# Performance work log

Measured on AMD Instinct MI355X. Metric: run time of the kernel, lower is better.

## Reference

```python
import jax, jax.numpy as jnp
import numpy as np

B = 32; H = 56; W = 56; C = 384; WS = 7; SHIFT = 3; NH = 12; HID = 1536; RANK = 192
N = WS * WS
NWIN = (H // WS) * (W // WS)


def _rel_index():
    coords = np.stack(np.meshgrid(np.arange(WS), np.arange(WS), indexing='ij')).reshape(2, -1)
    rel = (coords[:, :, None] - coords[:, None, :]).transpose(1, 2, 0)
    rel[..., 0] += WS - 1
    rel[..., 1] += WS - 1
    rel[..., 0] *= 2 * WS - 1
    return jnp.asarray(rel.sum(-1).reshape(-1))  # (N*N,) int


def _attn_mask():
    img = np.zeros((H, W))
    cnt = 0
    sls = (slice(0, -WS), slice(-WS, -SHIFT), slice(-SHIFT, None))
    for hs in sls:
        for ws_ in sls:
            img[hs, ws_] = cnt
            cnt += 1
    mw = img.reshape(H // WS, WS, W // WS, WS).transpose(0, 2, 1, 3).reshape(-1, N)
    am = mw[:, None, :] - mw[:, :, None]
    return jnp.asarray(np.where(am != 0, -100.0, 0.0).astype(np.float32))  # (nW,N,N)


REL_IDX = _rel_index()
ATTN_MASK = _attn_mask()


def _ln(x, g, b):
    m = x.mean(-1, keepdims=True)
    v = ((x - m) ** 2).mean(-1, keepdims=True)
    return (x - m) / jnp.sqrt(v + 1e-5) * g + b


def _flin(x, v, u, b):
    # FactorizedLinear: x @ V^T @ U^T + b
    return (x @ v.T) @ u.T + b


def setup_inputs() -> dict:
    key = jax.random.key(0)
    ks = jax.random.split(key, 12)
    def n(k, shape, s):
        return jax.random.normal(k, shape, jnp.float32) * s
    return {
        'x': jax.random.normal(ks[0], (B, H * W, C), jnp.float32),
        'norm1_g': jnp.ones((C,), jnp.float32), 'norm1_b': jnp.zeros((C,), jnp.float32),
        'rpb_table': n(ks[1], ((2 * WS - 1) ** 2, NH), 0.02),
        'qkv_v': n(ks[2], (RANK, C), 0.05), 'qkv_u': n(ks[3], (3 * C, RANK), 0.05),
        'qkv_b': jnp.zeros((3 * C,), jnp.float32),
        'proj_v': n(ks[4], (RANK, C), 0.05), 'proj_u': n(ks[5], (C, RANK), 0.05),
        'proj_b': jnp.zeros((C,), jnp.float32),
        'norm2_g': jnp.ones((C,), jnp.float32), 'norm2_b': jnp.zeros((C,), jnp.float32),
        'fc1_v': n(ks[6], (RANK, C), 0.05), 'fc1_u': n(ks[7], (HID, RANK), 0.05),
        'fc1_b': jnp.zeros((HID,), jnp.float32),
        'fc2_v': n(ks[8], (RANK, HID), 0.05), 'fc2_u': n(ks[9], (C, RANK), 0.05),
        'fc2_b': jnp.zeros((C,), jnp.float32),
    }


def reference(x, norm1_g, norm1_b, rpb_table, qkv_v, qkv_u, qkv_b,
              proj_v, proj_u, proj_b, norm2_g, norm2_b,
              fc1_v, fc1_u, fc1_b, fc2_v, fc2_u, fc2_b):
    hd = C // NH
    scale = hd ** -0.5
    shortcut = x
    y = _ln(x, norm1_g, norm1_b).reshape(B, H, W, C)
    y = jnp.roll(y, (-SHIFT, -SHIFT), axis=(1, 2))  # cyclic shift
    # window partition -> (B*nW, N, C)
    y = y.reshape(B, H // WS, WS, W // WS, WS, C).transpose(0, 1, 3, 2, 4, 5).reshape(-1, N, C)
    qkv = _flin(y, qkv_v, qkv_u, qkv_b).reshape(-1, N, 3, NH, hd).transpose(2, 0, 3, 1, 4)
    q, k, v = qkv[0] * scale, qkv[1], qkv[2]  # (B*nW, NH, N, hd)
    attn = jnp.einsum('bhnd,bhmd->bhnm', q, k)
    rpb = rpb_table[REL_IDX].reshape(N, N, NH).transpose(2, 0, 1)  # (NH,N,N)
    attn = attn + rpb[None]
    attn = attn.reshape(B, NWIN, NH, N, N) + ATTN_MASK[None, :, None]
    attn = jax.nn.softmax(attn, axis=-1).reshape(-1, NH, N, N)
    o = jnp.einsum('bhnm,bhmd->bhnd', attn, v).transpose(0, 2, 1, 3).reshape(-1, N, C)
    o = _flin(o, proj_v, proj_u, proj_b)
    # window reverse + reverse shift
    o = o.reshape(B, H // WS, W // WS, WS, WS, C).transpose(0, 1, 3, 2, 4, 5).reshape(B, H, W, C)
    o = jnp.roll(o, (SHIFT, SHIFT), axis=(1, 2)).reshape(B, H * W, C)
    x = shortcut + o
    z = _ln(x, norm2_g, norm2_b)
    z = jax.nn.gelu(_flin(z, fc1_v, fc1_u, fc1_b), approximate=False)
    z = _flin(z, fc2_v, fc2_u, fc2_b)
    return x + z
```

## Files before the change

kernel.cpp:

```cpp
#include <hip/hip_runtime.h>
#include <hip/hip_bf16.h>

using bf16 = __hip_bfloat16;
typedef __bf16 bf16x8 __attribute__((ext_vector_type(8)));
typedef __bf16 bf16x4v __attribute__((ext_vector_type(4)));
typedef float f32x4 __attribute__((ext_vector_type(4)));

#define MROWS 100352

__device__ __forceinline__ void async16(void* l, const void* g) {
    void* gg = const_cast<void*>(g);
    __builtin_amdgcn_global_load_lds((__attribute__((address_space(1))) void*)gg,
                                     (__attribute__((address_space(3))) void*)l, 16, 0, 0);
}

__device__ __forceinline__ float gelu_f(float x) {
    float u = x * fmaf(0.044715f * x, x, 1.0f);
    float e = __expf(-1.5957691216057308f * u);
    return x * __builtin_amdgcn_rcpf(1.0f + e);
}

struct Cvt8 { const float* s[8]; bf16* d[8]; int n[8]; };

__global__ __launch_bounds__(256) void cvt8_k(Cvt8 c) {
    int seg = blockIdx.y;
    int i4 = (blockIdx.x * 256 + threadIdx.x) * 4;
    if (i4 < c.n[seg]) {
        float4 v = *(const float4*)(c.s[seg] + i4);
        bf16* d = c.d[seg] + i4;
        d[0] = __float2bfloat16(v.x);
        d[1] = __float2bfloat16(v.y);
        d[2] = __float2bfloat16(v.z);
        d[3] = __float2bfloat16(v.w);
    }
}

__global__ __launch_bounds__(384) void wmerge_k(const float* __restrict__ u,
                                                const float* __restrict__ v,
                                                bf16* __restrict__ wm) {
    int o = blockIdx.x, i = threadIdx.x;
    const float* ur = u + o * 192;
    float acc = 0.f;
    for (int r = 0; r < 192; ++r) acc = fmaf(ur[r], v[r * 384 + i], acc);
    wm[o * 384 + i] = __float2bfloat16(acc);
}

__global__ __launch_bounds__(256) void u_reord_k(const float* __restrict__ U,
                                                 bf16* __restrict__ Ur) {
    int g = blockIdx.x * 256 + threadIdx.x;
    int lane = g & 63, w = (g >> 6) & 3, q = g >> 8;
    int kk = q % 6, hc = q / 6;
    int row = hc * 64 + w * 16 + (lane & 15);
    int col = kk * 32 + (lane >> 4) * 8;
    const float* src = U + (size_t)row * 192 + col;
    bf16* d = Ur + (size_t)g * 8;
#pragma unroll
    for (int e = 0; e < 8; ++e) d[e] = __float2bfloat16(src[e]);
}

__global__ __launch_bounds__(256) void v_reord_k(const float* __restrict__ V2,
                                                 bf16* __restrict__ Vr) {
    int g = blockIdx.x * 256 + threadIdx.x;
    int lane = g & 63;
    int r = g >> 6;
    int tn = r % 3; r /= 3;
    int w = r & 3; r >>= 2;
    int kk2 = r & 1;
    int hc = r >> 1;
    int row = w * 48 + tn * 16 + (lane & 15);
    int col = hc * 64 + kk2 * 32 + (lane >> 4) * 8;
    const float* src = V2 + (size_t)row * 1536 + col;
    bf16* d = Vr + (size_t)g * 8;
#pragma unroll
    for (int e = 0; e < 8; ++e) d[e] = __float2bfloat16(src[e]);
}

__global__ __launch_bounds__(256) void bias_pre_k(const float* __restrict__ rpbt,
                                                  float* __restrict__ biasf) {
    int wt = blockIdx.x / 12, h = blockIdx.x % 12;
    int t = threadIdx.x;
    int lane = t >> 2, tb = t & 3;
    int hi = lane >> 4, lo = lane & 15;
    int m = tb * 16 + lo;
    bool bH = (wt & 2) != 0, bW = (wt & 1) != 0;
    float* outb = biasf + (size_t)blockIdx.x * 4096;
    int mm = m < 49 ? m : 0;
    int i2 = mm / 7, j2 = mm % 7;
    int rm = (bH ? (i2 < 4 ? 1 : 2) : 0) * 3 + (bW ? (j2 < 4 ? 1 : 2) : 0);
#pragma unroll
    for (int ta = 0; ta < 4; ++ta) {
#pragma unroll
        for (int j = 0; j < 4; ++j) {
            int n = ta * 16 + hi * 4 + j;
            float v;
            if (n < 49 && m < 49) {
                int i1 = n / 7, j1 = n % 7;
                int rn = (bH ? (i1 < 4 ? 1 : 2) : 0) * 3 + (bW ? (j1 < 4 ? 1 : 2) : 0);
                v = rpbt[((i1 - i2 + 6) * 13 + (j1 - j2 + 6)) * 12 + h];
                if (rn != rm) v -= 100.0f;
            } else {
                v = -1e30f;
            }
            outb[(ta * 4 + j) * 256 + t] = v;
        }
    }
}

__global__ __launch_bounds__(256) void ln1_window_k(const float* __restrict__ x,
                                                    const float* __restrict__ g,
                                                    const float* __restrict__ bta,
                                                    bf16* __restrict__ ywin) {
    int wrow = blockIdx.x * 4 + (threadIdx.x >> 6);
    int lane = threadIdx.x & 63;
    int tok = wrow % 49, win = wrow / 49;
    int i = tok / 7, j = tok % 7;
    int wwi = win & 7, whi = (win >> 3) & 7, bi = win >> 6;
    int hs = (whi * 7 + i + 3) % 56;
    int ws_ = (wwi * 7 + j + 3) % 56;
    const float* xr = x + ((size_t)bi * 3136 + (size_t)hs * 56 + ws_) * 384;
    float v[6]; float s = 0.f, s2 = 0.f;
#pragma unroll
    for (int u = 0; u < 6; ++u) { float t = xr[lane + 64 * u]; v[u] = t; s += t; s2 += t * t; }
#pragma unroll
    for (int d = 1; d < 64; d <<= 1) { s += __shfl_xor(s, d); s2 += __shfl_xor(s2, d); }
    float mean = s * (1.0f / 384.0f);
    float var = s2 * (1.0f / 384.0f) - mean * mean;
    float rstd = rsqrtf(var + 1e-5f);
    bf16* yr = ywin + (size_t)wrow * 384;
#pragma unroll
    for (int u = 0; u < 6; ++u) {
        int c = lane + 64 * u;
        yr[c] = __float2bfloat16((v[u] - mean) * rstd * g[c] + bta[c]);
    }
}

__global__ __launch_bounds__(256) void resid_ln2_k(const float* __restrict__ x,
                                                   const bf16* __restrict__ proj,
                                                   const float* __restrict__ g,
                                                   const float* __restrict__ bta,
                                                   float* __restrict__ x2,
                                                   bf16* __restrict__ z) {
    int row = blockIdx.x * 4 + (threadIdx.x >> 6);
    int lane = threadIdx.x & 63;
    int bi = row / 3136; int hw = row % 3136;
    int h = hw / 56, w = hw % 56;
    int h2 = (h + 53) % 56, w2 = (w + 53) % 56;
    int prow = ((bi * 8 + h2 / 7) * 8 + w2 / 7) * 49 + (h2 % 7) * 7 + (w2 % 7);
    const float* xr = x + (size_t)row * 384;
    const bf16* pr = proj + (size_t)prow * 384;
    float* x2r = x2 + (size_t)row * 384;
    float v[6]; float s = 0.f, s2 = 0.f;
#pragma unroll
    for (int u = 0; u < 6; ++u) {
        int c = lane + 64 * u;
        float t = xr[c] + __bfloat162float(pr[c]);
        v[u] = t; s += t; s2 += t * t;
        x2r[c] = t;
    }
#pragma unroll
    for (int d = 1; d < 64; d <<= 1) { s += __shfl_xor(s, d); s2 += __shfl_xor(s2, d); }
    float mean = s * (1.0f / 384.0f);
    float var = s2 * (1.0f / 384.0f) - mean * mean;
    float rstd = rsqrtf(var + 1e-5f);
    bf16* zr = z + (size_t)row * 384;
#pragma unroll
    for (int u = 0; u < 6; ++u) {
        int c = lane + 64 * u;
        zr[c] = __float2bfloat16((v[u] - mean) * rstd * g[c] + bta[c]);
    }
}

__global__ __launch_bounds__(256) void attn_mfma_k(const bf16* __restrict__ qkv,
                                                   const float* __restrict__ biasf,
                                                   bf16* __restrict__ o) {
    __shared__ __align__(16) __bf16 vt_s[4][32 * 72];
    __shared__ __align__(16) __bf16 p_s[4][32 * 72];
    const int win = blockIdx.x;
    const int r = blockIdx.y;
    const int wave = threadIdx.x >> 6, lane = threadIdx.x & 63;
    const int lo = lane & 15, hi = lane >> 4;
    const int whi = (win >> 3) & 7, wwi = win & 7;
    const int wt = ((whi == 7) ? 2 : 0) + ((wwi == 7) ? 1 : 0);
    __bf16* vt_w = vt_s[wave];
    __bf16* p_w = p_s[wave];
    const int h = r * 4 + wave;
    const bf16* qbase = qkv + (size_t)win * 49 * 1152 + h * 32;
    const float* btile = biasf + (size_t)(wt * 12 + h) * 4096;
    bf16x8 zf = {};

    {
        int m = lane;
        bf16x8 vrow[4];
#pragma unroll
        for (int d8 = 0; d8 < 4; ++d8)
            vrow[d8] = (m < 49) ? *(const bf16x8*)(qbase + (size_t)m * 1152 + 768 + d8 * 8) : zf;
#pragma unroll
        for (int d8 = 0; d8 < 4; ++d8)
#pragma unroll
            for (int e = 0; e < 8; ++e)
                vt_w[(d8 * 8 + e) * 72 + m] = vrow[d8][e];
    }
    bf16x8 aq[4], bk[4];
    const int kq = hi * 8;
#pragma unroll
    for (int ta = 0; ta < 4; ++ta) {
        int n = ta * 16 + lo;
        aq[ta] = (n < 49) ? *(const bf16x8*)(qbase + (size_t)n * 1152 + kq) : zf;
        bk[ta] = (n < 49) ? *(const bf16x8*)(qbase + (size_t)n * 1152 + 384 + kq) : zf;
    }
    f32x4 acc[4][4] = {};
#pragma unroll
    for (int ta = 0; ta < 4; ++ta)
#pragma unroll
        for (int tb = 0; tb < 4; ++tb)
            acc[ta][tb] = __builtin_amdgcn_mfma_f32_16x16x32_bf16(aq[ta], bk[tb], acc[ta][tb], 0, 0, 0);
#pragma unroll
    for (int ta = 0; ta < 4; ++ta) {
#pragma unroll
        for (int j = 0; j < 4; ++j) {
            float4 b4 = *(const float4*)(btile + (ta * 4 + j) * 256 + lane * 4);
            acc[ta][0][j] = fmaf(acc[ta][0][j], 0.17677669529663687f, b4.x);
            acc[ta][1][j] = fmaf(acc[ta][1][j], 0.17677669529663687f, b4.y);
            acc[ta][2][j] = fmaf(acc[ta][2][j], 0.17677669529663687f, b4.z);
            acc[ta][3][j] = fmaf(acc[ta][3][j], 0.17677669529663687f, b4.w);
        }
    }
    bf16x8 vb[2][2];
#pragma unroll
    for (int kb = 0; kb < 2; ++kb)
#pragma unroll
        for (int tb = 0; tb < 2; ++tb)
            vb[kb][tb] = *(const bf16x8*)(vt_w + (tb * 16 + lo) * 72 + kb * 32 + hi * 8);

    f32x4 oacc[4][2] = {};
#pragma unroll
    for (int half = 0; half < 2; ++half) {
#pragma unroll
        for (int tq = 0; tq < 2; ++tq) {
            int ta = half * 2 + tq;
#pragma unroll
            for (int j = 0; j < 4; ++j) {
                float mx = fmaxf(fmaxf(acc[ta][0][j], acc[ta][1][j]),
                                 fmaxf(acc[ta][2][j], acc[ta][3][j]));
                mx = fmaxf(mx, __shfl_xor(mx, 1));
                mx = fmaxf(mx, __shfl_xor(mx, 2));
                mx = fmaxf(mx, __shfl_xor(mx, 4));
                mx = fmaxf(mx, __shfl_xor(mx, 8));
                float e0 = __expf(acc[ta][0][j] - mx);
                float e1 = __expf(acc[ta][1][j] - mx);
                float e2 = __expf(acc[ta][2][j] - mx);
                float e3 = __expf(acc[ta][3][j] - mx);
                float sm = e0 + e1 + e2 + e3;
                sm += __shfl_xor(sm, 1);
                sm += __shfl_xor(sm, 2);
                sm += __shfl_xor(sm, 4);
                sm += __shfl_xor(sm, 8);
                float inv = __builtin_amdgcn_rcpf(sm);
                int nl = tq * 16 + hi * 4 + j;
                p_w[nl * 72 + lo]      = (__bf16)(e0 * inv);
                p_w[nl * 72 + 16 + lo] = (__bf16)(e1 * inv);
                p_w[nl * 72 + 32 + lo] = (__bf16)(e2 * inv);
                p_w[nl * 72 + 48 + lo] = (__bf16)(e3 * inv);
            }
        }
#pragma unroll
        for (int kb = 0; kb < 2; ++kb) {
#pragma unroll
            for (int tq = 0; tq < 2; ++tq) {
                bf16x8 pa = *(const bf16x8*)(p_w + (tq * 16 + lo) * 72 + kb * 32 + hi * 8);
#pragma unroll
                for (int tb = 0; tb < 2; ++tb)
                    oacc[half * 2 + tq][tb] =
                        __builtin_amdgcn_mfma_f32_16x16x32_bf16(pa, vb[kb][tb], oacc[half * 2 + tq][tb], 0, 0, 0);
            }
        }
    }
    bf16* obase = o + (size_t)win * 49 * 384 + h * 32;
#pragma unroll
    for (int ta = 0; ta < 4; ++ta) {
#pragma unroll
        for (int j = 0; j < 4; ++j) {
            int n = ta * 16 + hi * 4 + j;
            if (n < 49) {
#pragma unroll
                for (int tb = 0; tb < 2; ++tb)
                    obase[(size_t)n * 384 + tb * 16 + lo] = __float2bfloat16(oacc[ta][tb][j]);
            }
        }
    }
}

template <int K, int N, int WN, int EPI>
__global__ __launch_bounds__(WN * 128, 8 - WN) void gemm_bt(const bf16* __restrict__ A,
                                                            const bf16* __restrict__ W,
                                                            const float* __restrict__ bias,
                                                            void* __restrict__ Cout) {
    constexpr int T = WN * 128;
    constexpr int BN = WN * 32;
    __shared__ __align__(16) bf16 lds_a[128 * 64];
    __shared__ __align__(16) bf16 lds_b[BN * 64];
    const int t = threadIdx.x;
    const int wave = t >> 6, lane = t & 63;
    const int gdx = gridDim.x;
    int flat = blockIdx.y * gdx + blockIdx.x;
    int q = (gdx * gridDim.y) >> 3;
    int work = (flat & 7) * q + (flat >> 3);
    const int n0 = (work % gdx) * BN, m0 = (work / gdx) * 128;
    const int wm = wave / WN, wn = wave % WN;
    const int fr = lane & 15, hi = lane >> 4;
    const int srow = t >> 3;
    const int gslot = (t & 7) ^ (srow & 7);
    const bf16* abase = A + (size_t)(m0 + srow) * K + gslot * 8;
    const bf16* bbase = W + (size_t)(n0 + srow) * K + gslot * 8;
    char* la = (char*)lds_a + t * 16;
    char* lb = (char*)lds_b + t * 16;
    const int fp = fr & 7;
    const char* ra0 = (const char*)lds_a + (wm * 64 + fr) * 128 + (hi ^ fp) * 16;
    const char* ra1 = (const char*)lds_a + (wm * 64 + fr) * 128 + ((4 + hi) ^ fp) * 16;
    const char* rb0 = (const char*)lds_b + (wn * 32 + fr) * 128 + (hi ^ fp) * 16;
    const char* rb1 = (const char*)lds_b + (wn * 32 + fr) * 128 + ((4 + hi) ^ fp) * 16;
    f32x4 acc[4][2] = {};
#pragma unroll
    for (int kt = 0; kt < K; kt += 64) {
        if (kt > 0) __syncthreads();
#pragma unroll
        for (int i = 0; i < 1024 / T; ++i)
            async16(la + i * T * 16, abase + (size_t)i * (T >> 3) * K + kt);
#pragma unroll
        for (int i = 0; i < BN * 8 / T; ++i)
            async16(lb + i * T * 16, bbase + (size_t)i * (T >> 3) * K + kt);
        __syncthreads();
        bf16x8 af[4], bfr[2];
#pragma unroll
        for (int mi = 0; mi < 4; ++mi) af[mi] = *(const bf16x8*)(ra0 + mi * 2048);
#pragma unroll
        for (int ni = 0; ni < 2; ++ni) bfr[ni] = *(const bf16x8*)(rb0 + ni * 2048);
#pragma unroll
        for (int mi = 0; mi < 4; ++mi)
#pragma unroll
            for (int ni = 0; ni < 2; ++ni)
                acc[mi][ni] = __builtin_amdgcn_mfma_f32_16x16x32_bf16(bfr[ni], af[mi], acc[mi][ni], 0, 0, 0);
#pragma unroll
        for (int mi = 0; mi < 4; ++mi) af[mi] = *(const bf16x8*)(ra1 + mi * 2048);
#pragma unroll
        for (int ni = 0; ni < 2; ++ni) bfr[ni] = *(const bf16x8*)(rb1 + ni * 2048);
#pragma unroll
        for (int mi = 0; mi < 4; ++mi)
#pragma unroll
            for (int ni = 0; ni < 2; ++ni)
                acc[mi][ni] = __builtin_amdgcn_mfma_f32_16x16x32_bf16(bfr[ni], af[mi], acc[mi][ni], 0, 0, 0);
    }
    const int rq4 = hi * 4;
    const int ncol = n0 + wn * 32 + rq4;
    const size_t cbase = (size_t)(m0 + wm * 64 + fr) * N + ncol;
    const float* pb = bias ? bias + ncol : nullptr;
#pragma unroll
    for (int mi = 0; mi < 4; ++mi) {
#pragma unroll
        for (int ni = 0; ni < 2; ++ni) {
            float v0 = acc[mi][ni][0], v1 = acc[mi][ni][1];
            float v2 = acc[mi][ni][2], v3 = acc[mi][ni][3];
            if (pb) {
                float4 b4 = *(const float4*)(pb + ni * 16);
                v0 += b4.x; v1 += b4.y; v2 += b4.z; v3 += b4.w;
            }
            if (EPI == 1) { v0 = gelu_f(v0); v1 = gelu_f(v1); v2 = gelu_f(v2); v3 = gelu_f(v3); }
            if (EPI == 2) {
                float4* p = (float4*)((float*)Cout + cbase + (size_t)mi * 16 * N + ni * 16);
                float4 o = *p;
                o.x += v0; o.y += v1; o.z += v2; o.w += v3;
                *p = o;
            } else {
                bf16x4v st = { (__bf16)v0, (__bf16)v1, (__bf16)v2, (__bf16)v3 };
                *(bf16x4v*)((bf16*)Cout + cbase + (size_t)mi * 16 * N + ni * 16) = st;
            }
        }
    }
}

__global__ __launch_bounds__(256, 3) void mlp_mid_k(const bf16* __restrict__ A,
                                                    const bf16* __restrict__ Ur,
                                                    const bf16* __restrict__ Vr,
                                                    const float* __restrict__ b1,
                                                    bf16* __restrict__ Cout) {
    __shared__ __align__(16) bf16 lds_a[64 * 192];
    __shared__ __align__(16) bf16 lds_h[2][64 * 72];
    const int t = threadIdx.x;
    const int wave = t >> 6, lane = t & 63;
    const int wn = wave;
    const int fr = lane & 15, hi = lane >> 4;
    const int fp = fr & 7;
    const int m0 = blockIdx.x * 64;
#pragma unroll
    for (int i = 0; i < 6; ++i) {
        int u = i * 256 + t;
        int row = u / 24, slot = u % 24;
        int gslot = slot ^ (row & 7);
        async16((char*)lds_a + u * 16, A + (size_t)(m0 + row) * 192 + gslot * 8);
    }

    const bf16* ubase = Ur + ((size_t)wn * 64 + lane) * 8;
    const bf16* vbase = Vr + ((size_t)wn * 3 * 64 + lane) * 8;
    bf16x8 buc[6], bun[6];
#pragma unroll
    for (int kk = 0; kk < 6; ++kk)
        buc[kk] = *(const bf16x8*)(ubase + (size_t)kk * 2048);
    __syncthreads();

    f32x4 acc2[4][3] = {};
#pragma unroll 1
    for (int hc = 0; hc < 24; ++hc) {
        bf16x8 bvc[2][3];
#pragma unroll
        for (int kk2 = 0; kk2 < 2; ++kk2)
#pragma unroll
            for (int tn = 0; tn < 3; ++tn)
                bvc[kk2][tn] = *(const bf16x8*)(vbase + (size_t)(hc * 2 + kk2) * 6144 + tn * 512);
        if (hc + 1 < 24) {
#pragma unroll
            for (int kk = 0; kk < 6; ++kk)
                bun[kk] = *(const bf16x8*)(ubase + (size_t)((hc + 1) * 6 + kk) * 2048);
        }
        f32x4 acc1[4] = {};
#pragma unroll
        for (int kk = 0; kk < 6; ++kk) {
            bf16x8 af[4];
#pragma unroll
            for (int mi = 0; mi < 4; ++mi) {
                int row = mi * 16 + fr;
                af[mi] = *(const bf16x8*)((const char*)lds_a + row * 384 + ((kk * 4 + hi) ^ fp) * 16);
            }
#pragma unroll
            for (int mi = 0; mi < 4; ++mi)
                acc1[mi] = __builtin_amdgcn_mfma_f32_16x16x32_bf16(buc[kk], af[mi], acc1[mi], 0, 0, 0);
        }
        {
            bf16* hbuf = lds_h[hc & 1];
            float4 b4 = *(const float4*)(b1 + hc * 64 + wn * 16 + hi * 4);
#pragma unroll
            for (int mi = 0; mi < 4; ++mi) {
                int mrow = mi * 16 + fr;
                float v0 = gelu_f(acc1[mi][0] + b4.x);
                float v1 = gelu_f(acc1[mi][1] + b4.y);
                float v2 = gelu_f(acc1[mi][2] + b4.z);
                float v3 = gelu_f(acc1[mi][3] + b4.w);
                bf16x4v st = { (__bf16)v0, (__bf16)v1, (__bf16)v2, (__bf16)v3 };
                *(bf16x4v*)(hbuf + mrow * 72 + wn * 16 + hi * 4) = st;
            }
        }
        __syncthreads();
        {
            const bf16* hbuf = lds_h[hc & 1];
#pragma unroll
            for (int kk2 = 0; kk2 < 2; ++kk2) {
                bf16x8 af2[4];
#pragma unroll
                for (int mi = 0; mi < 4; ++mi) {
                    int mrow = mi * 16 + fr;
                    af2[mi] = *(const bf16x8*)(hbuf + mrow * 72 + kk2 * 32 + hi * 8);
                }
#pragma unroll
                for (int mi = 0; mi < 4; ++mi)
#pragma unroll
                    for (int tn = 0; tn < 3; ++tn)
                        acc2[mi][tn] = __builtin_amdgcn_mfma_f32_16x16x32_bf16(bvc[kk2][tn], af2[mi], acc2[mi][tn], 0, 0, 0);
            }
        }
#pragma unroll
        for (int kk = 0; kk < 6; ++kk) buc[kk] = bun[kk];
    }
    const size_t cbase = (size_t)(m0 + fr) * 192 + wn * 48 + hi * 4;
#pragma unroll
    for (int mi = 0; mi < 4; ++mi) {
#pragma unroll
        for (int tn = 0; tn < 3; ++tn) {
            bf16x4v st = { (__bf16)acc2[mi][tn][0], (__bf16)acc2[mi][tn][1],
                           (__bf16)acc2[mi][tn][2], (__bf16)acc2[mi][tn][3] };
            *(bf16x4v*)(Cout + cbase + (size_t)mi * 16 * 192 + tn * 16) = st;
        }
    }
}

extern "C" void kernel_launch(void* const* d_in, const int* in_sizes, int n_in,
                              void* d_out, int out_size, void* d_ws, size_t ws_size,
                              hipStream_t stream) {
    const float* x      = (const float*)d_in[0];
    const float* n1g    = (const float*)d_in[1];
    const float* n1b    = (const float*)d_in[2];
    const float* rpbt   = (const float*)d_in[3];
    const float* qkv_v  = (const float*)d_in[4];
    const float* qkv_u  = (const float*)d_in[5];
    const float* qkv_b  = (const float*)d_in[6];
    const float* proj_v = (const float*)d_in[7];
    const float* proj_u = (const float*)d_in[8];
    const float* proj_b = (const float*)d_in[9];
    const float* n2g    = (const float*)d_in[10];
    const float* n2b    = (const float*)d_in[11];
    const float* fc1_v  = (const float*)d_in[12];
    const float* fc1_u  = (const float*)d_in[13];
    const float* fc1_b  = (const float*)d_in[14];
    const float* fc2_v  = (const float*)d_in[15];
    const float* fc2_u  = (const float*)d_in[16];
    const float* fc2_b  = (const float*)d_in[17];

    char* ws = (char*)d_ws;
    bf16* wb = (bf16*)ws;
    bf16* w_qkv_v  = wb;
    bf16* w_qkv_u  = wb + 73728;
    bf16* w_proj_v = wb + 294912;
    bf16* w_proj_u = wb + 368640;
    bf16* w_fc1_v  = wb + 442368;
    bf16* w_fc1_u  = wb + 516096;
    bf16* w_fc2_v  = wb + 811008;
    bf16* w_fc2_u  = wb + 1105920;
    bf16* w_proj_m = wb + 1179648;
    float* biasf   = (float*)(ws + 3145728);
    bf16* w_u_r    = (bf16*)(ws + 4194304);
    bf16* w_v_r    = (bf16*)(ws + 4784128);
    size_t off = (size_t)6 << 20;
    bf16* R1 = (bf16*)(ws + off); off += (size_t)MROWS * 1536 * 2;
    bf16* R2 = (bf16*)(ws + off); off += (size_t)MROWS * 384 * 2;
    bf16* R3 = (bf16*)(ws + off);
    float* out = (float*)d_out;

    Cvt8 c;
    c.s[0] = qkv_v;  c.d[0] = w_qkv_v;  c.n[0] = 73728;
    c.s[1] = qkv_u;  c.d[1] = w_qkv_u;  c.n[1] = 221184;
    c.s[2] = proj_v; c.d[2] = w_proj_v; c.n[2] = 73728;
    c.s[3] = proj_u; c.d[3] = w_proj_u; c.n[3] = 73728;
    c.s[4] = fc1_v;  c.d[4] = w_fc1_v;  c.n[4] = 73728;
    c.s[5] = fc1_u;  c.d[5] = w_fc1_u;  c.n[5] = 294912;
    c.s[6] = fc2_v;  c.d[6] = w_fc2_v;  c.n[6] = 294912;
    c.s[7] = fc2_u;  c.d[7] = w_fc2_u;  c.n[7] = 73728;
    cvt8_k<<<dim3(288, 8), 256, 0, stream>>>(c);
    bias_pre_k<<<48, 256, 0, stream>>>(rpbt, biasf);
    wmerge_k<<<384, 384, 0, stream>>>(proj_u, proj_v, w_proj_m);
    u_reord_k<<<144, 256, 0, stream>>>(fc1_u, w_u_r);
    v_reord_k<<<144, 256, 0, stream>>>(fc2_v, w_v_r);

    ln1_window_k<<<MROWS / 4, 256, 0, stream>>>(x, n1g, n1b, R2);
    gemm_bt<384, 192, 2, 0><<<dim3(3, 784), 256, 0, stream>>>(R2, w_qkv_v, nullptr, R3);
    gemm_bt<192, 1152, 4, 0><<<dim3(9, 784), 512, 0, stream>>>(R3, w_qkv_u, qkv_b, R1);
    attn_mfma_k<<<dim3(2048, 3), 256, 0, stream>>>(R1, biasf, R2);
    gemm_bt<384, 384, 4, 0><<<dim3(3, 784), 512, 0, stream>>>(R2, w_proj_m, proj_b, R1);
    resid_ln2_k<<<MROWS / 4, 256, 0, stream>>>(x, R1, n2g, n2b, out, R2);
    gemm_bt<384, 192, 2, 0><<<dim3(3, 784), 256, 0, stream>>>(R2, w_fc1_v, nullptr, R3);
    mlp_mid_k<<<1568, 256, 0, stream>>>(R3, w_u_r, w_v_r, fc1_b, R1);
    gemm_bt<192, 384, 4, 2><<<dim3(3, 784), 512, 0, stream>>>(R1, w_fc2_u, fc2_b, out);
}
```

Measured before the change: 721.7 us.

## Add fragment-reordered weight GEMM with direct global B loads and swizzled block order

Introduces gemm_rw, which reads weights from a pre-reordered fragment layout straight from global memory into registers and stages only A (64 rows) in LDS. It replaces gemm_bt for the qkv_u, proj-merged and fc2_u GEMMs, using smaller 64x128 tiles with a block-index remap meant to improve L2 locality. Weight prep kernels now write these fragment layouts, and the unused conversions are dropped. The goal is to cut LDS traffic and sync on B and raise occupancy, at the cost of more blocks and repeated global weight reads.

```diff
diff --git a/kernel.cpp b/kernel.cpp
--- a/kernel.cpp
+++ b/kernel.cpp
@@ -35,6 +35,25 @@
     }
 }
 
+template <int K, int N>
+__global__ __launch_bounds__(256) void w_reord_k(const float* __restrict__ W,
+                                                 bf16* __restrict__ Wr) {
+    constexpr int KS = K / 32;
+    int g = blockIdx.x * 256 + threadIdx.x;
+    if (g >= N * K / 8) return;
+    int lane = g & 63;
+    int r = g >> 6;
+    int nn = r & 1; r >>= 1;
+    int w = r & 3; r >>= 2;
+    int kk = r % KS, c = r / KS;
+    int row = c * 128 + w * 32 + nn * 16 + (lane & 15);
+    int col = kk * 32 + (lane >> 4) * 8;
+    const float* src = W + (size_t)row * K + col;
+    bf16* d = Wr + (size_t)g * 8;
+#pragma unroll
+    for (int e = 0; e < 8; ++e) d[e] = __float2bfloat16(src[e]);
+}
+
 __global__ __launch_bounds__(384) void wmerge_k(const float* __restrict__ u,
                                                 const float* __restrict__ v,
                                                 bf16* __restrict__ wm) {
@@ -42,7 +61,10 @@
     const float* ur = u + o * 192;
     float acc = 0.f;
     for (int r = 0; r < 192; ++r) acc = fmaf(ur[r], v[r * 384 + i], acc);
-    wm[o * 384 + i] = __float2bfloat16(acc);
+    int c = o >> 7, w = (o >> 5) & 3, nn = (o >> 4) & 1, frl = o & 15;
+    int kk = i >> 5, hi = (i >> 3) & 3, e = i & 7;
+    size_t fragid = (size_t)(c * 12 + kk) * 8 + w * 2 + nn;
+    wm[fragid * 512 + (hi * 16 + frl) * 8 + e] = __float2bfloat16(acc);
 }
 
 __global__ __launch_bounds__(256) void u_reord_k(const float* __restrict__ U,
@@ -378,6 +400,77 @@
     }
 }
 
+template <int K, int N, int EPI>
+__global__ __launch_bounds__(256, 6) void gemm_rw(const bf16* __restrict__ A,
+                                                  const bf16* __restrict__ Wr,
+                                                  const float* __restrict__ bias,
+                                                  void* __restrict__ Cout) {
+    constexpr int KS = K / 32;
+    constexpr int SL = K / 8;
+    __shared__ __align__(16) bf16 lds_a[64 * K];
+    const int t = threadIdx.x;
+    const int wn = t >> 6, lane = t & 63;
+    const int fr = lane & 15, hi = lane >> 4;
+    const int fp = fr & 7;
+    const int gdx = gridDim.x;
+    int flat = blockIdx.y * gdx + blockIdx.x;
+    int q = (gdx * gridDim.y) >> 3;
+    int work = (flat & 7) * q + (flat >> 3);
+    const int c = work % gdx;
+    const int m0 = (work / gdx) * 64;
+#pragma unroll
+    for (int i = 0; i < SL * 64 / 256; ++i) {
+        int u = i * 256 + t;
+        int row = u / SL, slot = u % SL;
+        int gslot = slot ^ (row & 7);
+        async16((char*)lds_a + u * 16, A + (size_t)(m0 + row) * K + gslot * 8);
+    }
+    const bf16* wbase = Wr + ((size_t)c * KS * 8 + wn * 2) * 512 + lane * 8;
+    __syncthreads();
+    f32x4 acc[4][2] = {};
+#pragma unroll
+    for (int kk = 0; kk < KS; ++kk) {
+        bf16x8 bu0 = *(const bf16x8*)(wbase + (size_t)kk * 4096);
+        bf16x8 bu1 = *(const bf16x8*)(wbase + (size_t)kk * 4096 + 512);
+        bf16x8 af[4];
+#pragma unroll
+        for (int mi = 0; mi < 4; ++mi) {
+            int row = mi * 16 + fr;
+            af[mi] = *(const bf16x8*)((const char*)lds_a + row * (K * 2) + ((kk * 4 + hi) ^ fp) * 16);
+        }
+#pragma unroll
+        for (int mi = 0; mi < 4; ++mi) {
+            acc[mi][0] = __builtin_amdgcn_mfma_f32_16x16x32_bf16(bu0, af[mi], acc[mi][0], 0, 0, 0);
+            acc[mi][1] = __builtin_amdgcn_mfma_f32_16x16x32_bf16(bu1, af[mi], acc[mi][1], 0, 0, 0);
+        }
+    }
+    const int ncol = c * 128 + wn * 32 + hi * 4;
+    const size_t cbase = (size_t)(m0 + fr) * N + ncol;
+    const float* pb = bias ? bias + ncol : nullptr;
+#pragma unroll
+    for (int mi = 0; mi < 4; ++mi) {
+#pragma unroll
+        for (int nn = 0; nn < 2; ++nn) {
+            float v0 = acc[mi][nn][0], v1 = acc[mi][nn][1];
+            float v2 = acc[mi][nn][2], v3 = acc[mi][nn][3];
+            if (pb) {
+                float4 b4 = *(const float4*)(pb + nn * 16);
+                v0 += b4.x; v1 += b4.y; v2 += b4.z; v3 += b4.w;
+            }
+            if (EPI == 1) { v0 = gelu_f(v0); v1 = gelu_f(v1); v2 = gelu_f(v2); v3 = gelu_f(v3); }
+            if (EPI == 2) {
+                float4* p = (float4*)((float*)Cout + cbase + (size_t)mi * 16 * N + nn * 16);
+                float4 o = *p;
+                o.x += v0; o.y += v1; o.z += v2; o.w += v3;
+                *p = o;
+            } else {
+                bf16x4v st = { (__bf16)v0, (__bf16)v1, (__bf16)v2, (__bf16)v3 };
+                *(bf16x4v*)((bf16*)Cout + cbase + (size_t)mi * 16 * N + nn * 16) = st;
+            }
+        }
+    }
+}
+
 __global__ __launch_bounds__(256, 3) void mlp_mid_k(const bf16* __restrict__ A,
                                                     const bf16* __restrict__ Ur,
                                                     const bf16* __restrict__ Vr,
@@ -398,7 +491,6 @@
         int gslot = slot ^ (row & 7);
         async16((char*)lds_a + u * 16, A + (size_t)(m0 + row) * 192 + gslot * 8);
     }
-
     const bf16* ubase = Ur + ((size_t)wn * 64 + lane) * 8;
     const bf16* vbase = Vr + ((size_t)wn * 3 * 64 + lane) * 8;
     bf16x8 buc[6], bun[6];
@@ -505,18 +597,14 @@
 
     char* ws = (char*)d_ws;
     bf16* wb = (bf16*)ws;
-    bf16* w_qkv_v  = wb;
-    bf16* w_qkv_u  = wb + 73728;
-    bf16* w_proj_v = wb + 294912;
-    bf16* w_proj_u = wb + 368640;
-    bf16* w_fc1_v  = wb + 442368;
-    bf16* w_fc1_u  = wb + 516096;
-    bf16* w_fc2_v  = wb + 811008;
-    bf16* w_fc2_u  = wb + 1105920;
-    bf16* w_proj_m = wb + 1179648;
-    float* biasf   = (float*)(ws + 3145728);
-    bf16* w_u_r    = (bf16*)(ws + 4194304);
-    bf16* w_v_r    = (bf16*)(ws + 4784128);
+    bf16* w_qkv_v   = wb;
+    bf16* w_fc1_v   = wb + 73728;
+    bf16* w_qkv_u_r = wb + 147456;
+    bf16* w_fc2_u_r = wb + 368640;
+    bf16* w_proj_mr = wb + 442368;
+    bf16* w_u_r     = wb + 589824;
+    bf16* w_v_r     = wb + 884736;
+    float* biasf    = (float*)(ws + 3145728);
     size_t off = (size_t)6 << 20;
     bf16* R1 = (bf16*)(ws + off); off += (size_t)MROWS * 1536 * 2;
     bf16* R2 = (bf16*)(ws + off); off += (size_t)MROWS * 384 * 2;
@@ -525,26 +613,28 @@
 
     Cvt8 c;
     c.s[0] = qkv_v;  c.d[0] = w_qkv_v;  c.n[0] = 73728;
-    c.s[1] = qkv_u;  c.d[1] = w_qkv_u;  c.n[1] = 221184;
-    c.s[2] = proj_v; c.d[2] = w_proj_v; c.n[2] = 73728;
-    c.s[3] = proj_u; c.d[3] = w_proj_u; c.n[3] = 73728;
-    c.s[4] = fc1_v;  c.d[4] = w_fc1_v;  c.n[4] = 73728;
-    c.s[5] = fc1_u;  c.d[5] = w_fc1_u;  c.n[5] = 294912;
-    c.s[6] = fc2_v;  c.d[6] = w_fc2_v;  c.n[6] = 294912;
-    c.s[7] = fc2_u;  c.d[7] = w_fc2_u;  c.n[7] = 73728;
-    cvt8_k<<<dim3(288, 8), 256, 0, stream>>>(c);
+    c.s[1] = fc1_v;  c.d[1] = w_fc1_v;  c.n[1] = 73728;
+    c.s[2] = qkv_v;  c.d[2] = w_qkv_v;  c.n[2] = 0;
+    c.s[3] = qkv_v;  c.d[3] = w_qkv_v;  c.n[3] = 0;
+    c.s[4] = qkv_v;  c.d[4] = w_qkv_v;  c.n[4] = 0;
+    c.s[5] = qkv_v;  c.d[5] = w_qkv_v;  c.n[5] = 0;
+    c.s[6] = qkv_v;  c.d[6] = w_qkv_v;  c.n[6] = 0;
+    c.s[7] = qkv_v;  c.d[7] = w_qkv_v;  c.n[7] = 0;
+    cvt8_k<<<dim3(72, 2), 256, 0, stream>>>(c);
     bias_pre_k<<<48, 256, 0, stream>>>(rpbt, biasf);
-    wmerge_k<<<384, 384, 0, stream>>>(proj_u, proj_v, w_proj_m);
+    wmerge_k<<<384, 384, 0, stream>>>(proj_u, proj_v, w_proj_mr);
+    w_reord_k<192, 1152><<<108, 256, 0, stream>>>(qkv_u, w_qkv_u_r);
+    w_reord_k<192, 384><<<36, 256, 0, stream>>>(fc2_u, w_fc2_u_r);
     u_reord_k<<<144, 256, 0, stream>>>(fc1_u, w_u_r);
     v_reord_k<<<144, 256, 0, stream>>>(fc2_v, w_v_r);
 
     ln1_window_k<<<MROWS / 4, 256, 0, stream>>>(x, n1g, n1b, R2);
     gemm_bt<384, 192, 2, 0><<<dim3(3, 784), 256, 0, stream>>>(R2, w_qkv_v, nullptr, R3);
-    gemm_bt<192, 1152, 4, 0><<<dim3(9, 784), 512, 0, stream>>>(R3, w_qkv_u, qkv_b, R1);
+    gemm_rw<192, 1152, 0><<<dim3(9, 1568), 256, 0, stream>>>(R3, w_qkv_u_r, qkv_b, R1);
     attn_mfma_k<<<dim3(2048, 3), 256, 0, stream>>>(R1, biasf, R2);
-    gemm_bt<384, 384, 4, 0><<<dim3(3, 784), 512, 0, stream>>>(R2, w_proj_m, proj_b, R1);
+    gemm_rw<384, 384, 0><<<dim3(3, 1568), 256, 0, stream>>>(R2, w_proj_mr, proj_b, R1);
     resid_ln2_k<<<MROWS / 4, 256, 0, stream>>>(x, R1, n2g, n2b, out, R2);
     gemm_bt<384, 192, 2, 0><<<dim3(3, 784), 256, 0, stream>>>(R2, w_fc1_v, nullptr, R3);
     mlp_mid_k<<<1568, 256, 0, stream>>>(R3, w_u_r, w_v_r, fc1_b, R1);
-    gemm_bt<192, 384, 4, 2><<<dim3(3, 784), 512, 0, stream>>>(R1, w_fc2_u, fc2_b, out);
-}
+    gemm_rw<192, 384, 2><<<dim3(3, 1568), 256, 0, stream>>>(R1, w_fc2_u_r, fc2_b, out);
+}
```

Measured after the change: 756.0 us. 1.05x slower.
